# Optimization experiments

Measured on AMD Instinct MI355X. Metric: run time of the kernel, lower is better.

The kernel has to match this reference:

```python
import jax, jax.numpy as jnp
import numpy as np


def setup_inputs() -> dict:
    key = jax.random.key(0)
    k1, k2, k3 = jax.random.split(key, 3)
    B, T, F, H = 4, 2048, 256, 8
    x = jax.random.normal(k1, (B, T, F), dtype=jnp.float32)
    W_qkv = jax.random.normal(k2, (F, H * F * 3), dtype=jnp.float32) * (1.0 / np.sqrt(F))
    b_qkv = jnp.zeros((H * F * 3,), dtype=jnp.float32)
    W_proj = jax.random.normal(k3, (H * F, F), dtype=jnp.float32) * (1.0 / np.sqrt(H * F))
    b_proj = jnp.zeros((F,), dtype=jnp.float32)
    return {"x": x, "W_qkv": W_qkv, "b_qkv": b_qkv, "W_proj": W_proj, "b_proj": b_proj}


def reference(x, W_qkv, b_qkv, W_proj, b_proj):
    # x: [B, T, F]; heads H = 8, per-head dim = F (full in_features per head)
    B, T, F = x.shape
    H = W_qkv.shape[1] // (F * 3)
    temperature = 1.0
    qkv = x @ W_qkv + b_qkv                      # [B, T, H*F*3]
    qkv = qkv.reshape(B, T, H, F, 3)
    qkv = jnp.transpose(qkv, (0, 2, 1, 3, 4))    # [B, H, T, F, 3]
    inv_sqrt_f = 1.0 / jnp.sqrt(jnp.asarray(F, x.dtype))
    q = qkv[..., 0] * inv_sqrt_f                 # note: BOTH q and k scaled
    k = qkv[..., 1] * inv_sqrt_f
    v = qkv[..., 2]
    scores = jnp.einsum('bhtf,bhsf->bhts', q, k) / temperature  # [B, H, T, T]
    weights = jax.nn.softmax(scores, axis=-1)
    out = jnp.einsum('bhts,bhsf->bhtf', weights, v)              # [B, H, T, F]
    out = jnp.transpose(out, (0, 2, 1, 3)).reshape(B, T, H * F)  # [B, T, H*F]
    return out @ W_proj + b_proj                                 # [B, T, F]
```

## Files before the change

kernel.cpp:

```cpp
#include <hip/hip_runtime.h>
#include <hip/hip_bf16.h>


typedef __attribute__((ext_vector_type(8))) short bf16x8;
typedef __attribute__((ext_vector_type(4))) short s16x4;
typedef __attribute__((ext_vector_type(4))) float f32x4;
typedef __attribute__((ext_vector_type(16))) float f32x16;
typedef __attribute__((ext_vector_type(4))) int i32x4;

#define MFMA16(a, b, c) __builtin_amdgcn_mfma_f32_16x16x32_bf16((a), (b), (c), 0, 0, 0)
#define MFMA32(a, b, c) __builtin_amdgcn_mfma_f32_32x32x16_bf16((a), (b), (c), 0, 0, 0)

static __device__ __forceinline__ short bf16_bits(float v) {
    __hip_bfloat16 h = __float2bfloat16(v);
    return reinterpret_cast<short&>(h);
}

static __device__ __forceinline__ unsigned pack_bf16(float lo, float hi) {
    unsigned a = (unsigned)(unsigned short)bf16_bits(lo);
    unsigned b = (unsigned)(unsigned short)bf16_bits(hi);
    return a | (b << 16);
}

static __device__ __forceinline__ void dma_lds16(const void* g, void* l) {
    __builtin_amdgcn_global_load_lds((const __attribute__((address_space(1))) unsigned int*)g,
                                     (__attribute__((address_space(3))) unsigned int*)l,
                                     16, 0, 0);
}

static __device__ __forceinline__ i32x4 cvt8(const float* __restrict__ src) {
    f32x4 a = *(const f32x4*)(src);
    f32x4 b = *(const f32x4*)(src + 4);
    union { short s[8]; i32x4 v; } u;
#pragma unroll
    for (int i = 0; i < 4; ++i) {
        u.s[i]     = bf16_bits(a[i]);
        u.s[i + 4] = bf16_bits(b[i]);
    }
    return u.v;
}

__global__ __launch_bounds__(256) void k_cvt_x(const float* __restrict__ in,
                                               __hip_bfloat16* __restrict__ out) {
    size_t i = ((size_t)blockIdx.x * 256 + threadIdx.x) * 8;
    *(i32x4*)(out + i) = cvt8(in + i);
}

__global__ __launch_bounds__(256) void k_transpose_qkvw(const float* __restrict__ in,
                                                        __hip_bfloat16* __restrict__ out) {
    __shared__ __hip_bfloat16 tile[32][33];
    int tx = threadIdx.x & 31;
    int ty = threadIdx.x >> 5;
    int c0 = blockIdx.x * 32, r0 = blockIdx.y * 32;
#pragma unroll
    for (int j = 0; j < 4; ++j)
        tile[ty + j * 8][tx] = __float2bfloat16(in[(size_t)(r0 + ty + j * 8) * 6144 + c0 + tx]);
    __syncthreads();
#pragma unroll
    for (int j = 0; j < 4; ++j) {
        int n = c0 + ty + j * 8;
        int h = n / 768, rem = n - h * 768;
        int f = rem / 3, c = rem - f * 3;
        int np = c * 2048 + h * 256 + f;
        out[(size_t)np * 256 + r0 + tx] = tile[tx][ty + j * 8];
    }
}

__global__ __launch_bounds__(256) void k_transpose(const float* __restrict__ in,
                                                   __hip_bfloat16* __restrict__ out,
                                                   int rows, int cols) {
    __shared__ __hip_bfloat16 tile[32][33];
    int tx = threadIdx.x & 31;
    int ty = threadIdx.x >> 5;
    int c0 = blockIdx.x * 32, r0 = blockIdx.y * 32;
#pragma unroll
    for (int j = 0; j < 4; ++j)
        tile[ty + j * 8][tx] = __float2bfloat16(in[(size_t)(r0 + ty + j * 8) * cols + c0 + tx]);
    __syncthreads();
#pragma unroll
    for (int j = 0; j < 4; ++j)
        out[(size_t)(c0 + ty + j * 8) * rows + r0 + tx] = tile[tx][ty + j * 8];
}

#define GS 32
__global__ __launch_bounds__(256) void k_gemm_qkv(const __hip_bfloat16* __restrict__ X,
                                                  const __hip_bfloat16* __restrict__ Wt,
                                                  const float* __restrict__ bias,
                                                  __hip_bfloat16* __restrict__ Q,
                                                  __hip_bfloat16* __restrict__ K,
                                                  __hip_bfloat16* __restrict__ Vt) {
    __shared__ __align__(16) short As[2][128 * GS];
    __shared__ __align__(16) short Bs[2][128 * GS];
    const int tid = threadIdx.x;
    const int m0 = blockIdx.y * 128, n0 = blockIdx.x * 128;
    const int w = tid >> 6, lane = tid & 63, l16 = lane & 15, quad = lane >> 4;
    const int wm = (w >> 1) * 64, wn = (w & 1) * 64;

    const int ci0 = (w * 2 + 0) * 64 + lane, ci1 = (w * 2 + 1) * 64 + lane;
    const int r0s = ci0 >> 2, c0s = (ci0 & 3) * 8;
    const int r1s = ci1 >> 2, c1s = (ci1 & 3) * 8;

    f32x4 acc[4][4];
#pragma unroll
    for (int mi = 0; mi < 4; ++mi)
#pragma unroll
        for (int ni = 0; ni < 4; ++ni) acc[mi][ni] = (f32x4){0.f, 0.f, 0.f, 0.f};

    dma_lds16(X + (size_t)(m0 + r0s) * 256 + c0s, &As[0][(w * 2 + 0) * 512]);
    dma_lds16(Wt + (size_t)(n0 + r0s) * 256 + c0s, &Bs[0][(w * 2 + 0) * 512]);
    dma_lds16(X + (size_t)(m0 + r1s) * 256 + c1s, &As[0][(w * 2 + 1) * 512]);
    dma_lds16(Wt + (size_t)(n0 + r1s) * 256 + c1s, &Bs[0][(w * 2 + 1) * 512]);

    for (int it = 0; it < 8; ++it) {
        const int cur = it & 1, nxt = cur ^ 1;
        if (it < 7) {
            const int k0 = (it + 1) * 32;
            dma_lds16(X + (size_t)(m0 + r0s) * 256 + k0 + c0s, &As[nxt][(w * 2 + 0) * 512]);
            dma_lds16(Wt + (size_t)(n0 + r0s) * 256 + k0 + c0s, &Bs[nxt][(w * 2 + 0) * 512]);
            dma_lds16(X + (size_t)(m0 + r1s) * 256 + k0 + c1s, &As[nxt][(w * 2 + 1) * 512]);
            dma_lds16(Wt + (size_t)(n0 + r1s) * 256 + k0 + c1s, &Bs[nxt][(w * 2 + 1) * 512]);
            asm volatile("s_waitcnt vmcnt(4)" ::: "memory");
        } else {
            asm volatile("s_waitcnt vmcnt(0)" ::: "memory");
        }
        __builtin_amdgcn_s_barrier();

        bf16x8 af[4], bfr[4];
#pragma unroll
        for (int mi = 0; mi < 4; ++mi)
            af[mi] = *(const bf16x8*)&As[cur][(wm + mi * 16 + l16) * GS + quad * 8];
#pragma unroll
        for (int ni = 0; ni < 4; ++ni)
            bfr[ni] = *(const bf16x8*)&Bs[cur][(wn + ni * 16 + l16) * GS + quad * 8];
#pragma unroll
        for (int mi = 0; mi < 4; ++mi)
#pragma unroll
            for (int ni = 0; ni < 4; ++ni)
                acc[mi][ni] = MFMA16(af[mi], bfr[ni], acc[mi][ni]);

        asm volatile("s_waitcnt lgkmcnt(0)" ::: "memory");
        __builtin_amdgcn_s_barrier();
    }

    const int c = n0 >> 11;
    if (c < 2) {
        __hip_bfloat16* dst = (c == 0) ? Q : K;
        const int h = ((n0 + wn) >> 8) & 7;
        const int fb = (n0 + wn) & 255;
        const int m_base = m0 + wm;
        const int b = m_base >> 11;
        short* ebuf = &As[0][0] + w * (16 * 68);
#pragma unroll
        for (int mi = 0; mi < 4; ++mi) {
#pragma unroll
            for (int ni = 0; ni < 4; ++ni) {
                float bv = bias[h * 768 + (fb + ni * 16 + l16) * 3 + c];
#pragma unroll
                for (int r = 0; r < 4; ++r)
                    ebuf[(quad * 4 + r) * 68 + ni * 16 + l16] =
                        bf16_bits((acc[mi][ni][r] + bv) * 0.0625f);
            }
            asm volatile("s_waitcnt lgkmcnt(0)" ::: "memory");
#pragma unroll
            for (int p = 0; p < 2; ++p) {
                int row = p * 8 + (lane >> 3), cc = lane & 7;
                i32x4 v = *(const i32x4*)&ebuf[row * 68 + cc * 8];
                int t = (m_base + mi * 16 + row) & 2047;
                *(i32x4*)(dst + ((size_t)(b * 8 + h) * 2048 + t) * 256 + fb + cc * 8) = v;
            }
            asm volatile("s_waitcnt lgkmcnt(0)" ::: "memory");
        }
    } else {
        const int pos = ((quad & 1) << 3) | ((quad >> 1) << 2);
#pragma unroll
        for (int mi = 0; mi < 4; ++mi) {
            int m = m0 + wm + mi * 16 + quad * 4;
            int b = m >> 11, t = m & 2047;
            size_t tcol = (size_t)(t & ~31) + ((mi & 1) << 4) + pos;
#pragma unroll
            for (int ni = 0; ni < 4; ++ni) {
                int np = n0 + wn + ni * 16 + l16;
                int h = (np >> 8) & 7, f = np & 255;
                float bv = bias[h * 768 + f * 3 + 2];
                s16x4 v;
#pragma unroll
                for (int r = 0; r < 4; ++r) v[r] = bf16_bits(acc[mi][ni][r] + bv);
                *(s16x4*)(Vt + ((size_t)(b * 8 + h) * 256 + f) * 2048 + tcol) = v;
            }
        }
    }
}

#define VSS 40
#define ES 40
__global__ __launch_bounds__(512) void k_flash(const __hip_bfloat16* __restrict__ Q,
                                               const __hip_bfloat16* __restrict__ K,
                                               const __hip_bfloat16* __restrict__ Vt,
                                               __hip_bfloat16* __restrict__ O) {
    __shared__ __align__(16) short Ks[2][32 * 256];
    __shared__ __align__(16) short Vs[2][256 * VSS];
    const int tid = threadIdx.x;
    const int w = tid >> 6, lane = tid & 63;
    const int l32 = lane & 31, hi = lane >> 5;

    const int id = blockIdx.x;
    const int slot = id >> 3;
    const int bh = (id & 7) * 4 + (slot & 3);
    const int q0 = (slot >> 2) * 256;

    const __hip_bfloat16* Qb = Q + (size_t)bh * 2048 * 256;
    const __hip_bfloat16* Kb = K + (size_t)bh * 2048 * 256;
    const __hip_bfloat16* Vb = Vt + (size_t)bh * 256 * 2048;

    bf16x8 qf[16];
    {
        const __hip_bfloat16* qrow_p = Qb + (size_t)(q0 + w * 32 + l32) * 256 + hi * 8;
#pragma unroll
        for (int kf = 0; kf < 16; ++kf) qf[kf] = *(const bf16x8*)(qrow_p + kf * 16);
    }

    f32x16 oacc[8];
#pragma unroll
    for (int nt = 0; nt < 8; ++nt)
#pragma unroll
        for (int r = 0; r < 16; ++r) oacc[nt][r] = 0.f;
    float lsum = 0.f;

    const int vrow = (tid >> 2);
    const int vcol = (tid & 3) * 8;

#pragma unroll
    for (int p = 0; p < 2; ++p) {
        int seg = w * 2 + p;
        int r = 2 * seg + hi;
        int clog = l32 ^ (r & 7);
        dma_lds16(Kb + (size_t)r * 256 + clog * 8, &Ks[0][seg * 512]);
    }
#pragma unroll
    for (int p = 0; p < 2; ++p) {
        int row = vrow + p * 128;
        *(i32x4*)&Vs[0][row * VSS + vcol] = *(const i32x4*)(Vb + (size_t)row * 2048 + vcol);
    }
    __syncthreads();

    const int s7 = l32 & 7;
    for (int it = 0; it < 64; ++it) {
        const int cur = it & 1, nxt = cur ^ 1;
        const bool more = it < 63;
        const int ktn = (it + 1) * 32;

        i32x4 vreg[2];
        if (more) {
#pragma unroll
            for (int p = 0; p < 2; ++p) {
                int seg = w * 2 + p;
                int r = 2 * seg + hi;
                int clog = l32 ^ (r & 7);
                dma_lds16(Kb + (size_t)(ktn + r) * 256 + clog * 8, &Ks[nxt][seg * 512]);
            }
#pragma unroll
            for (int p = 0; p < 2; ++p) {
                int row = vrow + p * 128;
                vreg[p] = *(const i32x4*)(Vb + (size_t)row * 2048 + ktn + vcol);
            }
        }

        f32x16 s;
#pragma unroll
        for (int r = 0; r < 16; ++r) s[r] = 0.f;
        const short* ksb = &Ks[cur][l32 * 256];
#pragma unroll
        for (int kf = 0; kf < 16; ++kf) {
            int g = kf * 2 + hi;
            bf16x8 kfr = *(const bf16x8*)&ksb[((g ^ s7) * 8)];
            s = MFMA32(kfr, qf[kf], s);
        }

#pragma unroll
        for (int kk = 0; kk < 2; ++kk) {
            unsigned ch[4];
#pragma unroll
            for (int c = 0; c < 4; ++c) {
                float e0 = __expf(s[8 * kk + 2 * c]);
                float e1 = __expf(s[8 * kk + 2 * c + 1]);
                lsum += e0 + e1;
                ch[c] = pack_bf16(e0, e1);
            }
            union { i32x4 i; bf16x8 v; } pf;
            pf.i = (i32x4){(int)ch[0], (int)ch[1], (int)ch[2], (int)ch[3]};

#pragma unroll
            for (int nt = 0; nt < 8; ++nt) {
                bf16x8 vf = *(const bf16x8*)&Vs[cur][(nt * 32 + l32) * VSS + kk * 16 + hi * 8];
                oacc[nt] = MFMA32(vf, pf.v, oacc[nt]);
            }
        }

        if (more) {
#pragma unroll
            for (int p = 0; p < 2; ++p) {
                int row = vrow + p * 128;
                *(i32x4*)&Vs[nxt][row * VSS + vcol] = vreg[p];
            }
        }
        __syncthreads();
    }

    lsum += __shfl_xor(lsum, 32);
    const float inv = 1.f / lsum;

    short* ebuf = &Ks[0][0] + w * (32 * ES);
    const int b = bh >> 3, hh = bh & 7;
#pragma unroll
    for (int nt = 0; nt < 8; ++nt) {
#pragma unroll
        for (int r = 0; r < 16; ++r) {
            int fl = (r & 3) + 8 * (r >> 2) + 4 * hi;
            ebuf[l32 * ES + fl] = bf16_bits(oacc[nt][r] * inv);
        }
        asm volatile("s_waitcnt lgkmcnt(0)" ::: "memory");
#pragma unroll
        for (int p = 0; p < 2; ++p) {
            i32x4 v = *(const i32x4*)&ebuf[(lane >> 1) * ES + (lane & 1) * 8 + p * 16];
            int t = q0 + w * 32 + (lane >> 1);
            __hip_bfloat16* dst =
                O + ((size_t)(b * 2048 + t) * 2048 + hh * 256 + nt * 32 + (lane & 1) * 8 + p * 16);
            *(i32x4*)dst = v;
        }
        asm volatile("s_waitcnt lgkmcnt(0)" ::: "memory");
    }
}

__global__ __launch_bounds__(256) void k_gemm_proj(const __hip_bfloat16* __restrict__ A,
                                                   const __hip_bfloat16* __restrict__ Wt,
                                                   const float* __restrict__ bias,
                                                   float* __restrict__ Out) {
    __shared__ __align__(16) short As[2][128 * GS];
    __shared__ __align__(16) short Bs[2][64 * GS];
    const int tid = threadIdx.x;
    const int m0 = blockIdx.y * 128, n0 = blockIdx.x * 64;
    const int w = tid >> 6, lane = tid & 63, l16 = lane & 15, quad = lane >> 4;
    const int wm = w * 32;

    const int ciA0 = (w * 2 + 0) * 64 + lane, ciA1 = (w * 2 + 1) * 64 + lane;
    const int rA0 = ciA0 >> 2, cA0 = (ciA0 & 3) * 8;
    const int rA1 = ciA1 >> 2, cA1 = (ciA1 & 3) * 8;
    const int ciB = w * 64 + lane;
    const int rB = ciB >> 2, cB = (ciB & 3) * 8;

    f32x4 acc[2][4];
#pragma unroll
    for (int mi = 0; mi < 2; ++mi)
#pragma unroll
        for (int ni = 0; ni < 4; ++ni) acc[mi][ni] = (f32x4){0.f, 0.f, 0.f, 0.f};

    dma_lds16(A + (size_t)(m0 + rA0) * 2048 + cA0, &As[0][(w * 2 + 0) * 512]);
    dma_lds16(A + (size_t)(m0 + rA1) * 2048 + cA1, &As[0][(w * 2 + 1) * 512]);
    dma_lds16(Wt + (size_t)(n0 + rB) * 2048 + cB, &Bs[0][w * 512]);

    for (int it = 0; it < 64; ++it) {
        const int cur = it & 1, nxt = cur ^ 1;
        if (it < 63) {
            const int k0 = (it + 1) * 32;
            dma_lds16(A + (size_t)(m0 + rA0) * 2048 + k0 + cA0, &As[nxt][(w * 2 + 0) * 512]);
            dma_lds16(A + (size_t)(m0 + rA1) * 2048 + k0 + cA1, &As[nxt][(w * 2 + 1) * 512]);
            dma_lds16(Wt + (size_t)(n0 + rB) * 2048 + k0 + cB, &Bs[nxt][w * 512]);
            asm volatile("s_waitcnt vmcnt(3)" ::: "memory");
        } else {
            asm volatile("s_waitcnt vmcnt(0)" ::: "memory");
        }
        __builtin_amdgcn_s_barrier();

        bf16x8 af[2], bfr[4];
#pragma unroll
        for (int mi = 0; mi < 2; ++mi)
            af[mi] = *(const bf16x8*)&As[cur][(wm + mi * 16 + l16) * GS + quad * 8];
#pragma unroll
        for (int ni = 0; ni < 4; ++ni)
            bfr[ni] = *(const bf16x8*)&Bs[cur][(ni * 16 + l16) * GS + quad * 8];
#pragma unroll
        for (int mi = 0; mi < 2; ++mi)
#pragma unroll
            for (int ni = 0; ni < 4; ++ni)
                acc[mi][ni] = MFMA16(af[mi], bfr[ni], acc[mi][ni]);

        asm volatile("s_waitcnt lgkmcnt(0)" ::: "memory");
        __builtin_amdgcn_s_barrier();
    }

#pragma unroll
    for (int mi = 0; mi < 2; ++mi)
#pragma unroll
        for (int ni = 0; ni < 4; ++ni) {
            int n = n0 + ni * 16 + l16;
            float bv = bias[n];
#pragma unroll
            for (int r = 0; r < 4; ++r) {
                int m = m0 + wm + mi * 16 + quad * 4 + r;
                Out[(size_t)m * 256 + n] = acc[mi][ni][r] + bv;
            }
        }
}

extern "C" void kernel_launch(void* const* d_in, const int* in_sizes, int n_in,
                              void* d_out, int out_size, void* d_ws, size_t ws_size,
                              hipStream_t stream) {
    const float* x      = (const float*)d_in[0];
    const float* W_qkv  = (const float*)d_in[1];
    const float* b_qkv  = (const float*)d_in[2];
    const float* W_proj = (const float*)d_in[3];
    const float* b_proj = (const float*)d_in[4];
    float* out = (float*)d_out;

    const size_t E = 32ull * 2048 * 256;
    __hip_bfloat16* Qb     = (__hip_bfloat16*)d_ws;
    __hip_bfloat16* Kb     = Qb + E;
    __hip_bfloat16* Vt     = Kb + E;
    __hip_bfloat16* attn   = Vt + E;
    __hip_bfloat16* WqkvT  = attn + E;
    __hip_bfloat16* WprojT = WqkvT + 6144 * 256;
    __hip_bfloat16* Xb     = attn;

    k_cvt_x<<<dim3(8192 * 256 / (256 * 8)), 256, 0, stream>>>(x, Xb);
    k_transpose_qkvw<<<dim3(6144 / 32, 256 / 32), 256, 0, stream>>>(W_qkv, WqkvT);
    k_transpose<<<dim3(256 / 32, 2048 / 32), 256, 0, stream>>>(W_proj, WprojT, 2048, 256);
    k_gemm_qkv<<<dim3(48, 64), 256, 0, stream>>>(Xb, WqkvT, b_qkv, Qb, Kb, Vt);
    k_flash<<<dim3(256), 512, 0, stream>>>(Qb, Kb, Vt, attn);
    k_gemm_proj<<<dim3(4, 64), 256, 0, stream>>>(attn, WprojT, b_proj, out);
}
```

Baseline: 295.2 us.

## Merge preprocessing kernels and shrink projection GEMM tiles to 64x64

Folds the x conversion and both weight transposes into a single launch that dispatches on block index, removing two kernel launches. The projection GEMM moves from 128x64 tiles (256 blocks) to 64x64 tiles (512 blocks), with a block ordering that groups M tiles sharing the same N slice. This is meant to fill the 256 CUs more fully in the projection. In exchange, each block reuses less data per loaded tile and issues fewer MFMAs per barrier.

```diff
diff --git a/kernel.cpp b/kernel.cpp
--- a/kernel.cpp
+++ b/kernel.cpp
@@ -40,46 +40,49 @@
     return u.v;
 }
 
-__global__ __launch_bounds__(256) void k_cvt_x(const float* __restrict__ in,
-                                               __hip_bfloat16* __restrict__ out) {
-    size_t i = ((size_t)blockIdx.x * 256 + threadIdx.x) * 8;
-    *(i32x4*)(out + i) = cvt8(in + i);
-}
-
-__global__ __launch_bounds__(256) void k_transpose_qkvw(const float* __restrict__ in,
-                                                        __hip_bfloat16* __restrict__ out) {
+__global__ __launch_bounds__(256) void k_pre(const float* __restrict__ x,
+                                             const float* __restrict__ W_qkv,
+                                             const float* __restrict__ W_proj,
+                                             __hip_bfloat16* __restrict__ Xb,
+                                             __hip_bfloat16* __restrict__ WqkvT,
+                                             __hip_bfloat16* __restrict__ WprojT) {
+    const int id = blockIdx.x;
+    if (id < 1024) {
+        size_t i = ((size_t)id * 256 + threadIdx.x) * 8;
+        *(i32x4*)(Xb + i) = cvt8(x + i);
+        return;
+    }
     __shared__ __hip_bfloat16 tile[32][33];
-    int tx = threadIdx.x & 31;
-    int ty = threadIdx.x >> 5;
-    int c0 = blockIdx.x * 32, r0 = blockIdx.y * 32;
-#pragma unroll
-    for (int j = 0; j < 4; ++j)
-        tile[ty + j * 8][tx] = __float2bfloat16(in[(size_t)(r0 + ty + j * 8) * 6144 + c0 + tx]);
-    __syncthreads();
-#pragma unroll
-    for (int j = 0; j < 4; ++j) {
-        int n = c0 + ty + j * 8;
-        int h = n / 768, rem = n - h * 768;
-        int f = rem / 3, c = rem - f * 3;
-        int np = c * 2048 + h * 256 + f;
-        out[(size_t)np * 256 + r0 + tx] = tile[tx][ty + j * 8];
-    }
-}
-
-__global__ __launch_bounds__(256) void k_transpose(const float* __restrict__ in,
-                                                   __hip_bfloat16* __restrict__ out,
-                                                   int rows, int cols) {
-    __shared__ __hip_bfloat16 tile[32][33];
-    int tx = threadIdx.x & 31;
-    int ty = threadIdx.x >> 5;
-    int c0 = blockIdx.x * 32, r0 = blockIdx.y * 32;
-#pragma unroll
-    for (int j = 0; j < 4; ++j)
-        tile[ty + j * 8][tx] = __float2bfloat16(in[(size_t)(r0 + ty + j * 8) * cols + c0 + tx]);
-    __syncthreads();
-#pragma unroll
-    for (int j = 0; j < 4; ++j)
-        out[(size_t)(c0 + ty + j * 8) * rows + r0 + tx] = tile[tx][ty + j * 8];
+    const int tx = threadIdx.x & 31;
+    const int ty = threadIdx.x >> 5;
+    if (id < 2560) {
+        const int t = id - 1024;
+        const int c0 = (t % 192) * 32, r0 = (t / 192) * 32;
+#pragma unroll
+        for (int j = 0; j < 4; ++j)
+            tile[ty + j * 8][tx] =
+                __float2bfloat16(W_qkv[(size_t)(r0 + ty + j * 8) * 6144 + c0 + tx]);
+        __syncthreads();
+#pragma unroll
+        for (int j = 0; j < 4; ++j) {
+            int n = c0 + ty + j * 8;
+            int h = n / 768, rem = n - h * 768;
+            int f = rem / 3, c = rem - f * 3;
+            int np = c * 2048 + h * 256 + f;
+            WqkvT[(size_t)np * 256 + r0 + tx] = tile[tx][ty + j * 8];
+        }
+    } else {
+        const int t = id - 2560;
+        const int c0 = (t & 7) * 32, r0 = (t >> 3) * 32;
+#pragma unroll
+        for (int j = 0; j < 4; ++j)
+            tile[ty + j * 8][tx] =
+                __float2bfloat16(W_proj[(size_t)(r0 + ty + j * 8) * 256 + c0 + tx]);
+        __syncthreads();
+#pragma unroll
+        for (int j = 0; j < 4; ++j)
+            WprojT[(size_t)(c0 + ty + j * 8) * 2048 + r0 + tx] = tile[tx][ty + j * 8];
+    }
 }
 
 #define GS 32
@@ -335,71 +338,60 @@
                                                    const __hip_bfloat16* __restrict__ Wt,
                                                    const float* __restrict__ bias,
                                                    float* __restrict__ Out) {
-    __shared__ __align__(16) short As[2][128 * GS];
+    __shared__ __align__(16) short As[2][64 * GS];
     __shared__ __align__(16) short Bs[2][64 * GS];
     const int tid = threadIdx.x;
-    const int m0 = blockIdx.y * 128, n0 = blockIdx.x * 64;
+    const int id = blockIdx.x;
+    const int slot = id >> 3;
+    const int n0 = (slot & 3) * 64;
+    const int m0 = ((id & 7) + 8 * (slot >> 2)) * 64;
     const int w = tid >> 6, lane = tid & 63, l16 = lane & 15, quad = lane >> 4;
-    const int wm = w * 32;
-
-    const int ciA0 = (w * 2 + 0) * 64 + lane, ciA1 = (w * 2 + 1) * 64 + lane;
-    const int rA0 = ciA0 >> 2, cA0 = (ciA0 & 3) * 8;
-    const int rA1 = ciA1 >> 2, cA1 = (ciA1 & 3) * 8;
-    const int ciB = w * 64 + lane;
-    const int rB = ciB >> 2, cB = (ciB & 3) * 8;
-
-    f32x4 acc[2][4];
-#pragma unroll
-    for (int mi = 0; mi < 2; ++mi)
-#pragma unroll
-        for (int ni = 0; ni < 4; ++ni) acc[mi][ni] = (f32x4){0.f, 0.f, 0.f, 0.f};
-
-    dma_lds16(A + (size_t)(m0 + rA0) * 2048 + cA0, &As[0][(w * 2 + 0) * 512]);
-    dma_lds16(A + (size_t)(m0 + rA1) * 2048 + cA1, &As[0][(w * 2 + 1) * 512]);
-    dma_lds16(Wt + (size_t)(n0 + rB) * 2048 + cB, &Bs[0][w * 512]);
+    const int wm = w * 16;
+
+    const int rS = tid >> 2, cS = (tid & 3) * 8;
+
+    f32x4 acc[4];
+#pragma unroll
+    for (int ni = 0; ni < 4; ++ni) acc[ni] = (f32x4){0.f, 0.f, 0.f, 0.f};
+
+    dma_lds16(A + (size_t)(m0 + rS) * 2048 + cS, &As[0][w * 512]);
+    dma_lds16(Wt + (size_t)(n0 + rS) * 2048 + cS, &Bs[0][w * 512]);
 
     for (int it = 0; it < 64; ++it) {
         const int cur = it & 1, nxt = cur ^ 1;
         if (it < 63) {
             const int k0 = (it + 1) * 32;
-            dma_lds16(A + (size_t)(m0 + rA0) * 2048 + k0 + cA0, &As[nxt][(w * 2 + 0) * 512]);
-            dma_lds16(A + (size_t)(m0 + rA1) * 2048 + k0 + cA1, &As[nxt][(w * 2 + 1) * 512]);
-            dma_lds16(Wt + (size_t)(n0 + rB) * 2048 + k0 + cB, &Bs[nxt][w * 512]);
-            asm volatile("s_waitcnt vmcnt(3)" ::: "memory");
+            dma_lds16(A + (size_t)(m0 + rS) * 2048 + k0 + cS, &As[nxt][w * 512]);
+            dma_lds16(Wt + (size_t)(n0 + rS) * 2048 + k0 + cS, &Bs[nxt][w * 512]);
+            asm volatile("s_waitcnt vmcnt(2)" ::: "memory");
         } else {
             asm volatile("s_waitcnt vmcnt(0)" ::: "memory");
         }
         __builtin_amdgcn_s_barrier();
 
-        bf16x8 af[2], bfr[4];
-#pragma unroll
-        for (int mi = 0; mi < 2; ++mi)
-            af[mi] = *(const bf16x8*)&As[cur][(wm + mi * 16 + l16) * GS + quad * 8];
+        bf16x8 af = *(const bf16x8*)&As[cur][(wm + l16) * GS + quad * 8];
+        bf16x8 bfr[4];
 #pragma unroll
         for (int ni = 0; ni < 4; ++ni)
             bfr[ni] = *(const bf16x8*)&Bs[cur][(ni * 16 + l16) * GS + quad * 8];
 #pragma unroll
-        for (int mi = 0; mi < 2; ++mi)
-#pragma unroll
-            for (int ni = 0; ni < 4; ++ni)
-                acc[mi][ni] = MFMA16(af[mi], bfr[ni], acc[mi][ni]);
+        for (int ni = 0; ni < 4; ++ni)
+            acc[ni] = MFMA16(af, bfr[ni], acc[ni]);
 
         asm volatile("s_waitcnt lgkmcnt(0)" ::: "memory");
         __builtin_amdgcn_s_barrier();
     }
 
 #pragma unroll
-    for (int mi = 0; mi < 2; ++mi)
-#pragma unroll
-        for (int ni = 0; ni < 4; ++ni) {
-            int n = n0 + ni * 16 + l16;
-            float bv = bias[n];
-#pragma unroll
-            for (int r = 0; r < 4; ++r) {
-                int m = m0 + wm + mi * 16 + quad * 4 + r;
-                Out[(size_t)m * 256 + n] = acc[mi][ni][r] + bv;
-            }
-        }
+    for (int ni = 0; ni < 4; ++ni) {
+        int n = n0 + ni * 16 + l16;
+        float bv = bias[n];
+#pragma unroll
+        for (int r = 0; r < 4; ++r) {
+            int m = m0 + wm + quad * 4 + r;
+            Out[(size_t)m * 256 + n] = acc[ni][r] + bv;
+        }
+    }
 }
 
 extern "C" void kernel_launch(void* const* d_in, const int* in_sizes, int n_in,
@@ -421,10 +413,8 @@
     __hip_bfloat16* WprojT = WqkvT + 6144 * 256;
     __hip_bfloat16* Xb     = attn;
 
-    k_cvt_x<<<dim3(8192 * 256 / (256 * 8)), 256, 0, stream>>>(x, Xb);
-    k_transpose_qkvw<<<dim3(6144 / 32, 256 / 32), 256, 0, stream>>>(W_qkv, WqkvT);
-    k_transpose<<<dim3(256 / 32, 2048 / 32), 256, 0, stream>>>(W_proj, WprojT, 2048, 256);
+    k_pre<<<dim3(3072), 256, 0, stream>>>(x, W_qkv, W_proj, Xb, WqkvT, WprojT);
     k_gemm_qkv<<<dim3(48, 64), 256, 0, stream>>>(Xb, WqkvT, b_qkv, Qb, Kb, Vt);
     k_flash<<<dim3(256), 512, 0, stream>>>(Qb, Kb, Vt, attn);
-    k_gemm_proj<<<dim3(4, 64), 256, 0, stream>>>(attn, WprojT, b_proj, out);
-}
+    k_gemm_proj<<<dim3(512), 256, 0, stream>>>(attn, WprojT, b_proj, out);
+}
```

Measured after the change: 290.3 us (median of 2 runs). About the same (-1.7%).
